# Performance work log

Hardware: AMD Instinct MI355X
Metric: run time of the kernel (lower is better)

Reference implementation:

```python
import jax, jax.numpy as jnp
import numpy as np

N_NODES = 40000
N_EDGES = 640000
N_GRAPHS = 64
F_IN = 32       # fourier_order*4
D_EMB = 256     # int(0.5*512)
D_HID = 512     # int(0.5*1024)
D_FC = 1024     # int(0.5*2048)
N_CLS = 10


def setup_inputs() -> dict:
    key = jax.random.key(0)
    ks = iter(jax.random.split(key, 40))
    rn = lambda shape, s=0.05: jax.random.normal(next(ks), shape, jnp.float32) * s
    inp = {
        'x': jax.random.normal(next(ks), (N_NODES, F_IN), jnp.float32),
        'edge_index': jax.random.randint(next(ks), (2, N_EDGES), 0, N_NODES, jnp.int32),
        'edge_attr': jax.random.uniform(next(ks), (N_EDGES, 1), jnp.float32),
        'batch': jnp.sort(jax.random.randint(next(ks), (N_NODES,), 0, N_GRAPHS, jnp.int32)),
        # embedding MLP
        'emb_w1': rn((F_IN, D_EMB)), 'emb_b1': jnp.zeros((D_EMB,), jnp.float32),
        'emb_w2': rn((D_EMB, D_EMB)), 'emb_b2': jnp.zeros((D_EMB,), jnp.float32),
        # edge_proj MLP
        'ep_w1': rn((1, 64)), 'ep_b1': jnp.zeros((64,), jnp.float32),
        'ep_w2': rn((64, 1)), 'ep_b2': jnp.zeros((1,), jnp.float32),
        # GCNConv weights (x @ W + b, PyG convention)
        'w_c1': rn((D_EMB, D_HID)), 'b_c1': jnp.zeros((D_HID,), jnp.float32),
        'w_c2': rn((D_HID, D_HID)), 'b_c2': jnp.zeros((D_HID,), jnp.float32),
        'w_c3': rn((D_HID, D_HID)), 'b_c3': jnp.zeros((D_HID,), jnp.float32),
        'w_c4': rn((D_HID, D_HID)), 'b_c4': jnp.zeros((D_HID,), jnp.float32),
        'w_c5': rn((D_HID, D_HID)), 'b_c5': jnp.zeros((D_HID,), jnp.float32),
        'w_c6': rn((D_HID, D_HID)), 'b_c6': jnp.zeros((D_HID,), jnp.float32),
        # head
        'fc1_w': rn((D_HID, D_FC)), 'fc1_b': jnp.zeros((D_FC,), jnp.float32),
        'head_w': rn((D_FC, N_CLS)), 'head_b': jnp.zeros((N_CLS,), jnp.float32),
    }
    return inp


def _gcn_conv(x, src, dst, norm, W, b):
    # PyG GCNConv: linear transform, then normalized scatter-add aggregation, then bias
    h = x @ W                                   # [N, d_out]
    msg = h[src] * norm[:, None]                # [E+N, d_out] gathered messages
    agg = jax.ops.segment_sum(msg, dst, num_segments=N_NODES)
    return agg + b


def _forward(x, edge_attr, emb_w1, emb_b1, emb_w2, emb_b2, ep_w1, ep_b1, ep_w2, ep_b2,
             w_c1, b_c1, w_c2, b_c2, w_c3, b_c3, w_c4, b_c4, w_c5, b_c5, w_c6, b_c6,
             fc1_w, fc1_b, head_w, head_b, edge_index, batch):
    # edge weights from edge_proj MLP (sigmoid output in (0,1))
    ew = jax.nn.sigmoid(jax.nn.relu(edge_attr @ ep_w1 + ep_b1) @ ep_w2 + ep_b2)[:, 0]  # [E]
    # gcn_norm with self loops (identical for every conv layer -> compute once)
    loops = jnp.arange(N_NODES, dtype=edge_index.dtype)
    src = jnp.concatenate([edge_index[0], loops])
    dst = jnp.concatenate([edge_index[1], loops])
    w = jnp.concatenate([ew, jnp.ones((N_NODES,), ew.dtype)])
    deg = jax.ops.segment_sum(w, dst, num_segments=N_NODES)
    dinv = jnp.where(deg > 0, jax.lax.rsqrt(jnp.maximum(deg, 1e-12)), 0.0)
    norm = dinv[src] * w * dinv[dst]            # [E+N]

    h = jax.nn.relu(jax.nn.relu(x @ emb_w1 + emb_b1) @ emb_w2 + emb_b2)
    h = _gcn_conv(h, src, dst, norm, w_c1, b_c1)
    skip = jax.nn.relu(h)
    h = _gcn_conv(skip, src, dst, norm, w_c2, b_c2)
    h = jax.nn.relu(h)
    h = _gcn_conv(h, src, dst, norm, w_c3, b_c3)
    skip = jax.nn.relu(h) + skip                # has_skip=True
    h = _gcn_conv(skip, src, dst, norm, w_c4, b_c4)  # is_deep=True
    h = jax.nn.relu(h)
    h = _gcn_conv(h, src, dst, norm, w_c5, b_c5)
    h = jax.nn.relu(h)
    h = _gcn_conv(h, src, dst, norm, w_c6, b_c6)
    skip = jax.nn.relu(h) + skip

    # global mean pool over graphs
    sums = jax.ops.segment_sum(skip, batch, num_segments=N_GRAPHS)
    cnts = jax.ops.segment_sum(jnp.ones((N_NODES,), skip.dtype), batch, num_segments=N_GRAPHS)
    pooled = sums / jnp.maximum(cnts, 1.0)[:, None]   # [G, D_HID]

    out = jax.nn.relu(pooled @ fc1_w + fc1_b) @ head_w + head_b   # [G, N_CLS]
    return out


def reference(x, edge_index, edge_attr, batch, emb_w1, emb_b1, emb_w2, emb_b2,
              ep_w1, ep_b1, ep_w2, ep_b2, w_c1, b_c1, w_c2, b_c2, w_c3, b_c3,
              w_c4, b_c4, w_c5, b_c5, w_c6, b_c6, fc1_w, fc1_b, head_w, head_b):
    return _forward(x, edge_attr, emb_w1, emb_b1, emb_w2, emb_b2, ep_w1, ep_b1, ep_w2, ep_b2,
                    w_c1, b_c1, w_c2, b_c2, w_c3, b_c3, w_c4, b_c4, w_c5, b_c5, w_c6, b_c6,
                    fc1_w, fc1_b, head_w, head_b, edge_index, batch)
```

## Files before the change

### kernel.cpp

```cpp
#include <hip/hip_runtime.h>
#include <math.h>

#define N_NODES 40000
#define MP      40192
#define NROWB   157
#define N_EDGES 640000
#define N_GRAPHS 64
#define F_IN 32
#define D_EMB 256
#define D_HID 512
#define D_FC 1024
#define N_CLS 10

typedef _Float16 f16x8 __attribute__((ext_vector_type(8)));
typedef float f32x4  __attribute__((ext_vector_type(4)));
typedef unsigned short u16;

template <int N> struct VecU;
template <> struct VecU<2> { typedef unsigned T __attribute__((ext_vector_type(2))); };
template <> struct VecU<4> { typedef unsigned T __attribute__((ext_vector_type(4))); };

__device__ __forceinline__ float h2f(u16 u) {
    union { u16 s; _Float16 h; } v; v.s = u; return (float)v.h;
}
__device__ __forceinline__ u16 f2h(float f) {
    union { u16 s; _Float16 h; } v; v.h = (_Float16)f; return v.s;
}
__device__ __forceinline__ void async16(void* lds, const void* g) {
    __builtin_amdgcn_global_load_lds((const __attribute__((address_space(1))) void*)g,
                                     (__attribute__((address_space(3))) void*)lds, 16, 0, 0);
}

__global__ void prep_all(const float* __restrict__ x, u16* __restrict__ xb, u16* __restrict__ G,
                         float* __restrict__ deg, int* __restrict__ cnt, int* __restrict__ cursor,
                         float* __restrict__ sums) {
    int i = blockIdx.x * blockDim.x + threadIdx.x;
    if (i < N_NODES) { deg[i] = 1.0f; cnt[i] = 0; cursor[i] = 0; }
    if (i < MP * F_IN) {
        int row = i >> 5;
        xb[i] = (row < N_NODES) ? f2h(x[i]) : (u16)0;
    }
    if (i < (MP - N_NODES) * D_HID) G[(size_t)N_NODES * D_HID + i] = 0;
    if (i < N_GRAPHS * D_HID) sums[i] = 0.f;
}

__global__ void edge_mlp_deg(const float* __restrict__ edge_attr,
                             const float* __restrict__ ep_w1, const float* __restrict__ ep_b1,
                             const float* __restrict__ ep_w2, const float* __restrict__ ep_b2,
                             const int* __restrict__ dst,
                             float* __restrict__ ew, float* __restrict__ deg, int* __restrict__ cnt) {
    __shared__ float w1[64], b1[64], w2[64];
    int t = threadIdx.x;
    if (t < 64) { w1[t] = ep_w1[t]; b1[t] = ep_b1[t]; w2[t] = ep_w2[t]; }
    __syncthreads();
    int e = blockIdx.x * blockDim.x + t;
    if (e >= N_EDGES) return;
    float x = edge_attr[e];
    float s = ep_b2[0];
#pragma unroll
    for (int j = 0; j < 64; ++j) s += fmaxf(x * w1[j] + b1[j], 0.f) * w2[j];
    float sig = 1.f / (1.f + expf(-s));
    ew[e] = sig;
    int d = dst[e];
    atomicAdd(&deg[d], sig);
    atomicAdd(&cnt[d], 1);
}

__global__ void dinv_kernel(const float* __restrict__ deg, float* __restrict__ dinv,
                            float* __restrict__ nloop) {
    int i = blockIdx.x * blockDim.x + threadIdx.x;
    if (i >= N_NODES) return;
    float d = deg[i];
    float r = (d > 0.f) ? rsqrtf(fmaxf(d, 1e-12f)) : 0.f;
    dinv[i] = r;
    nloop[i] = r * r;
}

__global__ void scan_kernel(const int* __restrict__ cnt, int* __restrict__ rowptr) {
    __shared__ int part[1024];
    int t = threadIdx.x;
    const int PER = (N_NODES + 1023) / 1024;
    int base = t * PER;
    int s = 0;
    for (int k = 0; k < PER; ++k) { int i = base + k; if (i < N_NODES) s += cnt[i]; }
    part[t] = s;
    __syncthreads();
    for (int off = 1; off < 1024; off <<= 1) {
        int v = (t >= off) ? part[t - off] : 0;
        __syncthreads();
        part[t] += v;
        __syncthreads();
    }
    int run = (t == 0) ? 0 : part[t - 1];
    for (int k = 0; k < PER; ++k) {
        int i = base + k;
        if (i < N_NODES) { rowptr[i] = run; run += cnt[i]; }
    }
    if (t == 1023) rowptr[N_NODES] = run;
}

__global__ void fill_csr_kernel(const int* __restrict__ src, const int* __restrict__ dst,
                                const float* __restrict__ ew, const float* __restrict__ dinv,
                                const int* __restrict__ rowptr, int* __restrict__ cursor,
                                int2* __restrict__ cv) {
    int e = blockIdx.x * blockDim.x + threadIdx.x;
    if (e >= N_EDGES) return;
    int d = dst[e];
    int s = src[e];
    float n = dinv[s] * ew[e] * dinv[d];
    int p = rowptr[d] + atomicAdd(&cursor[d], 1);
    cv[p] = make_int2(s, __float_as_int(n));
}

struct WPair { const float* s; u16* d; int K; int N; };
struct WP8 { WPair m[8]; };

__global__ void wprep_all(WP8 a) {
    __shared__ u16 th[32][33];
    WPair w = a.m[blockIdx.z];
    int n0 = blockIdx.x * 32;
    int k0 = blockIdx.y * 32;
    if (n0 >= w.N || k0 >= w.K) return;
    int tx = threadIdx.x, ty = threadIdx.y;
#pragma unroll
    for (int r = 0; r < 4; ++r) {
        int k = ty + r * 8;
        th[k][tx] = f2h(w.s[(size_t)(k0 + k) * w.N + n0 + tx]);
    }
    __syncthreads();
#pragma unroll
    for (int r = 0; r < 4; ++r) {
        int n = ty + r * 8;
        w.d[(size_t)(n0 + n) * w.K + k0 + tx] = th[tx][n];
    }
}

__launch_bounds__(512)
__global__ void mfma_gemm(const u16* __restrict__ A,
                          const u16* __restrict__ W,
                          const float* __restrict__ bias,
                          const u16* __restrict__ skip,
                          u16* __restrict__ C, int K, int N,
                          const int* __restrict__ batch, float* __restrict__ pool) {
    __shared__ __align__(16) u16 smem[2 * 12288];
    __shared__ int sbatch[128];

    int nColB = N >> 7;
    int b = blockIdx.x;
    int rowI = (b >> 3) / nColB * 8 + (b & 7);
    int colI = (b >> 3) % nColB;
    if (rowI >= NROWB) return;
    int rowBase = rowI * 256;
    int colBase = colI * 128;

    int t = threadIdx.x;
    int lane = t & 63;
    int wave = t >> 6;
    int wr = wave >> 1;
    int wc = wave & 1;

    int tt  = (lane & 7) ^ ((lane >> 3) & 7);
    int rrl = ((lane >> 3) << 1) | (tt >> 2);
    int sel = (tt & 3) * 8;
    int r0A = wave * 32;
    int r0W = wave * 16;

    int quad = lane >> 4;
    int mrow = lane & 15;

    const u16* gA = A + (size_t)(rowBase + r0A + rrl) * K + sel;
    const u16* gW = W + (size_t)(colBase + r0W + rrl) * K + sel;

    f32x4 acc[4][4] = {};

    int nIter = K >> 5;
    {
        u16* As = smem; u16* Ws = smem + 8192;
        async16(&As[r0A * 32], gA);
        async16(&As[(r0A + 16) * 32], gA + (size_t)16 * K);
        async16(&Ws[r0W * 32], gW);
    }

    for (int it = 0; it < nIter; ++it) {
        int cur = it & 1;
        __syncthreads();
        if (it + 1 < nIter) {
            int k0 = (it + 1) << 5;
            u16* As = smem + (cur ^ 1) * 12288; u16* Ws = As + 8192;
            async16(&As[r0A * 32], gA + k0);
            async16(&As[(r0A + 16) * 32], gA + k0 + (size_t)16 * K);
            async16(&Ws[r0W * 32], gW + k0);
        }
        const u16* As = smem + cur * 12288;
        const u16* Ws = As + 8192;
        f16x8 af[4], wf[4];
#pragma unroll
        for (int i = 0; i < 4; ++i) {
            int Ra = wr * 64 + i * 16 + mrow;
            int sa = ((Ra & 1) * 4 + quad) ^ ((Ra >> 1) & 7);
            af[i] = *(const f16x8*)&As[(Ra >> 1) * 64 + sa * 8];
            int Rb = wc * 64 + i * 16 + mrow;
            int sb = ((Rb & 1) * 4 + quad) ^ ((Rb >> 1) & 7);
            wf[i] = *(const f16x8*)&Ws[(Rb >> 1) * 64 + sb * 8];
        }
#pragma unroll
        for (int i = 0; i < 4; ++i)
#pragma unroll
            for (int j = 0; j < 4; ++j)
                acc[i][j] = __builtin_amdgcn_mfma_f32_16x16x32_f16(af[i], wf[j], acc[i][j], 0, 0, 0);
    }
    __syncthreads();

    const int ES = 132;
    u16* eb = smem;
#pragma unroll
    for (int ph = 0; ph < 2; ++ph) {
        if ((wr >> 1) == ph) {
#pragma unroll
            for (int j = 0; j < 4; ++j) {
                int col = colBase + wc * 64 + j * 16 + mrow;
                float bv = bias[col];
#pragma unroll
                for (int i = 0; i < 4; ++i) {
#pragma unroll
                    for (int r = 0; r < 4; ++r) {
                        int lr = (wr & 1) * 64 + i * 16 + quad * 4 + r;
                        size_t row = (size_t)rowBase + ph * 128 + lr;
                        float v = fmaxf(acc[i][j][r] + bv, 0.f);
                        if (skip) v += h2f(skip[row * N + col]);
                        eb[lr * ES + wc * 64 + j * 16 + mrow] = f2h(v);
                    }
                }
            }
        }
        if (pool && t < 128) {
            int row = rowBase + ph * 128 + t;
            sbatch[t] = (row < N_NODES) ? batch[row] : -1;
        }
        __syncthreads();
        if (C) {
#pragma unroll
            for (int k = 0; k < 4; ++k) {
                int c = t + k * 512;
                int row = c >> 4;
                int ch = c & 15;
                f16x8 v = *(const f16x8*)&eb[row * ES + ch * 8];
                __builtin_nontemporal_store(v,
                    (f16x8*)&C[(size_t)(rowBase + ph * 128 + row) * N + colBase + ch * 8]);
            }
        }
        if (pool) {
            int c = t & 127;
            int rs = (t >> 7) * 32;
            float run = 0.f; int g = -1;
            for (int r = rs; r < rs + 32; ++r) {
                int bg = sbatch[r];
                if (bg != g) {
                    if (g >= 0) atomicAdd(&pool[(size_t)g * D_HID + colBase + c], run);
                    run = 0.f; g = bg;
                }
                if (bg >= 0) run += h2f(eb[r * ES + c]);
            }
            if (g >= 0) atomicAdd(&pool[(size_t)g * D_HID + colBase + c], run);
        }
        __syncthreads();
    }
}

template <int D>
__launch_bounds__(256)
__global__ void gather_f16(const u16* __restrict__ h, const int* __restrict__ rowptr,
                           const int2* __restrict__ cv, const float* __restrict__ nloop,
                           u16* __restrict__ out) {
    constexpr int FPL = D / 64;
    constexpr int UPL = FPL / 2;
    using VU = typename VecU<UPL>::T;
    int node = blockIdx.x * 4 + (threadIdx.x >> 6);
    int lane = threadIdx.x & 63;
    if (node >= N_NODES) return;
    union UU { unsigned u; _Float16 h[2]; };
    float acc[FPL];
    float sl = nloop[node];
    {
        VU own = *(const VU*)(h + (size_t)node * D + lane * FPL);
#pragma unroll
        for (int u = 0; u < UPL; ++u) {
            UU w; w.u = own[u];
            acc[2 * u]     = (float)w.h[0] * sl;
            acc[2 * u + 1] = (float)w.h[1] * sl;
        }
    }
    int beg = rowptr[node], end = rowptr[node + 1];
    if (end > beg) {
        int last = end - 1;
        int2 c[8];
#pragma unroll
        for (int m = 0; m < 8; ++m) c[m] = cv[min(beg + m, last)];
        for (int j = beg; j < end; j += 8) {
            VU tv[8];
#pragma unroll
            for (int m = 0; m < 8; ++m)
                tv[m] = *(const VU*)(h + (size_t)c[m].x * D + lane * FPL);
            int jn = j + 8;
            int2 cn[8];
#pragma unroll
            for (int m = 0; m < 8; ++m) cn[m] = c[m];
            if (jn < end) {
#pragma unroll
                for (int m = 0; m < 8; ++m) cn[m] = cv[min(jn + m, last)];
            }
            __builtin_amdgcn_sched_barrier(0);
#pragma unroll
            for (int m = 0; m < 8; ++m) {
                float v = (j + m < end) ? __int_as_float(c[m].y) : 0.f;
#pragma unroll
                for (int u = 0; u < UPL; ++u) {
                    UU w; w.u = tv[m][u];
                    acc[2 * u]     += (float)w.h[0] * v;
                    acc[2 * u + 1] += (float)w.h[1] * v;
                }
            }
#pragma unroll
            for (int m = 0; m < 8; ++m) c[m] = cn[m];
        }
    }
    VU o;
#pragma unroll
    for (int u = 0; u < UPL; ++u) {
        unsigned lo = f2h(acc[2 * u]);
        unsigned hi = f2h(acc[2 * u + 1]);
        o[u] = lo | (hi << 16);
    }
    __builtin_nontemporal_store(o, (VU*)(out + (size_t)node * D + lane * FPL));
}

__launch_bounds__(256)
__global__ void fc1_head(const float* __restrict__ sums, const int* __restrict__ batch,
                         const float* __restrict__ fc1_w, const float* __restrict__ fc1_b,
                         const float* __restrict__ head_w, const float* __restrict__ head_b,
                         float* __restrict__ out) {
    __shared__ float sv[D_HID];
    __shared__ float fj[D_FC];
    __shared__ float hacc[N_CLS];
    __shared__ float invc;
    int g = blockIdx.x;
    int t = threadIdx.x;
    if (t == 0) {
        int lo = 0, hi = N_NODES;
        while (lo < hi) { int m = (lo + hi) >> 1; if (batch[m] < g) lo = m + 1; else hi = m; }
        int lb = lo;
        lo = lb; hi = N_NODES;
        while (lo < hi) { int m = (lo + hi) >> 1; if (batch[m] < g + 1) lo = m + 1; else hi = m; }
        invc = 1.f / fmaxf((float)(lo - lb), 1.f);
    }
    if (t < N_CLS) hacc[t] = 0.f;
    __syncthreads();
    for (int k = t; k < D_HID; k += 256) sv[k] = sums[(size_t)g * D_HID + k] * invc;
    __syncthreads();
#pragma unroll
    for (int m = 0; m < D_FC / 256; ++m) {
        int j = t + m * 256;
        float acc = fc1_b[j];
        for (int k = 0; k < D_HID; ++k) acc += sv[k] * fc1_w[(size_t)k * D_FC + j];
        fj[j] = fmaxf(acc, 0.f);
    }
    __syncthreads();
    float p[N_CLS] = {};
    for (int j = t; j < D_FC; j += 256) {
        float f = fj[j];
#pragma unroll
        for (int c = 0; c < N_CLS; ++c) p[c] += f * head_w[j * N_CLS + c];
    }
#pragma unroll
    for (int c = 0; c < N_CLS; ++c) {
        float v = p[c];
        for (int off = 32; off; off >>= 1) v += __shfl_down(v, off, 64);
        if ((t & 63) == 0) atomicAdd(&hacc[c], v);
    }
    __syncthreads();
    if (t < N_CLS) out[g * N_CLS + t] = hacc[t] + head_b[t];
}

extern "C" void kernel_launch(void* const* d_in, const int* in_sizes, int n_in,
                              void* d_out, int out_size, void* d_ws, size_t ws_size,
                              hipStream_t stream) {
    const float* x          = (const float*)d_in[0];
    const int*   edge_index = (const int*)d_in[1];
    const float* edge_attr  = (const float*)d_in[2];
    const int*   batch      = (const int*)d_in[3];
    const float* emb_w1 = (const float*)d_in[4];
    const float* emb_b1 = (const float*)d_in[5];
    const float* emb_w2 = (const float*)d_in[6];
    const float* emb_b2 = (const float*)d_in[7];
    const float* ep_w1  = (const float*)d_in[8];
    const float* ep_b1  = (const float*)d_in[9];
    const float* ep_w2  = (const float*)d_in[10];
    const float* ep_b2  = (const float*)d_in[11];
    const float* w_c[6] = { (const float*)d_in[12], (const float*)d_in[14], (const float*)d_in[16],
                            (const float*)d_in[18], (const float*)d_in[20], (const float*)d_in[22] };
    const float* b_c[6] = { (const float*)d_in[13], (const float*)d_in[15], (const float*)d_in[17],
                            (const float*)d_in[19], (const float*)d_in[21], (const float*)d_in[23] };
    const float* fc1_w  = (const float*)d_in[24];
    const float* fc1_b  = (const float*)d_in[25];
    const float* head_w = (const float*)d_in[26];
    const float* head_b = (const float*)d_in[27];
    float* out = (float*)d_out;

    const int* src = edge_index;
    const int* dst = edge_index + N_EDGES;

    char* p = (char*)d_ws;
    auto alloc = [&](size_t bytes) { char* r = p; p += (bytes + 255) & ~(size_t)255; return r; };
    float* ew    = (float*)alloc(N_EDGES * 4);
    float* deg   = (float*)alloc(N_NODES * 4);
    float* dinv  = (float*)alloc(N_NODES * 4);
    float* nloop = (float*)alloc(N_NODES * 4);
    int* cnt     = (int*)alloc(N_NODES * 4);
    int* cursor  = (int*)alloc(N_NODES * 4);
    int* rowptr  = (int*)alloc((N_NODES + 1) * 4);
    int2* cv     = (int2*)alloc((size_t)N_EDGES * 8);
    u16* xb = (u16*)alloc((size_t)MP * F_IN * 2);
    u16* H1 = (u16*)alloc((size_t)MP * D_EMB * 2);
    u16* H2 = (u16*)alloc((size_t)MP * D_EMB * 2);
    u16* G  = (u16*)alloc((size_t)MP * D_HID * 2);
    u16* S1 = (u16*)alloc((size_t)MP * D_HID * 2);
    u16* S2 = (u16*)alloc((size_t)MP * D_HID * 2);
    u16* Cb = (u16*)alloc((size_t)MP * D_HID * 2);
    u16* we1 = (u16*)alloc((size_t)F_IN * D_EMB * 2);
    u16* we2 = (u16*)alloc((size_t)D_EMB * D_EMB * 2);
    u16* wc[6];
    wc[0] = (u16*)alloc((size_t)D_EMB * D_HID * 2);
    for (int i = 1; i < 6; ++i) wc[i] = (u16*)alloc((size_t)D_HID * D_HID * 2);
    float* sums = (float*)alloc(N_GRAPHS * D_HID * 4);

    const int TB = 256;
    const int EB = (N_EDGES + TB - 1) / TB;
    const int NB = (N_NODES + TB - 1) / TB;

    prep_all<<<(MP * F_IN + TB - 1) / TB, TB, 0, stream>>>(x, xb, G, deg, cnt, cursor, sums);
    edge_mlp_deg<<<EB, TB, 0, stream>>>(edge_attr, ep_w1, ep_b1, ep_w2, ep_b2, dst, ew, deg, cnt);
    dinv_kernel<<<NB, TB, 0, stream>>>(deg, dinv, nloop);
    scan_kernel<<<1, 1024, 0, stream>>>(cnt, rowptr);
    fill_csr_kernel<<<EB, TB, 0, stream>>>(src, dst, ew, dinv, rowptr, cursor, cv);

    WP8 wp;
    wp.m[0] = { emb_w1, we1, F_IN,  D_EMB };
    wp.m[1] = { emb_w2, we2, D_EMB, D_EMB };
    wp.m[2] = { w_c[0], wc[0], D_EMB, D_HID };
    for (int i = 1; i < 6; ++i) wp.m[2 + i] = { w_c[i], wc[i], D_HID, D_HID };
    wprep_all<<<dim3(16, 16, 8), dim3(32, 8), 0, stream>>>(wp);

    const int SLOTS = ((NROWB + 7) / 8) * 8;
    const int GRID2 = SLOTS * (D_EMB / 128);
    const int GRID4 = SLOTS * (D_HID / 128);
    mfma_gemm<<<GRID2, 512, 0, stream>>>(xb, we1, emb_b1, nullptr, H1, F_IN, D_EMB, nullptr, nullptr);
    mfma_gemm<<<GRID2, 512, 0, stream>>>(H1, we2, emb_b2, nullptr, H2, D_EMB, D_EMB, nullptr, nullptr);

    const int GG = (N_NODES + 3) / 4;
    gather_f16<D_EMB><<<GG, 256, 0, stream>>>(H2, rowptr, cv, nloop, G);
    mfma_gemm<<<GRID4, 512, 0, stream>>>(G, wc[0], b_c[0], nullptr, S1, D_EMB, D_HID, nullptr, nullptr);
    gather_f16<D_HID><<<GG, 256, 0, stream>>>(S1, rowptr, cv, nloop, G);
    mfma_gemm<<<GRID4, 512, 0, stream>>>(G, wc[1], b_c[1], nullptr, Cb, D_HID, D_HID, nullptr, nullptr);
    gather_f16<D_HID><<<GG, 256, 0, stream>>>(Cb, rowptr, cv, nloop, G);
    mfma_gemm<<<GRID4, 512, 0, stream>>>(G, wc[2], b_c[2], S1, S2, D_HID, D_HID, nullptr, nullptr);
    gather_f16<D_HID><<<GG, 256, 0, stream>>>(S2, rowptr, cv, nloop, G);
    mfma_gemm<<<GRID4, 512, 0, stream>>>(G, wc[3], b_c[3], nullptr, Cb, D_HID, D_HID, nullptr, nullptr);
    gather_f16<D_HID><<<GG, 256, 0, stream>>>(Cb, rowptr, cv, nloop, G);
    mfma_gemm<<<GRID4, 512, 0, stream>>>(G, wc[4], b_c[4], nullptr, Cb, D_HID, D_HID, nullptr, nullptr);
    gather_f16<D_HID><<<GG, 256, 0, stream>>>(Cb, rowptr, cv, nloop, G);
    mfma_gemm<<<GRID4, 512, 0, stream>>>(G, wc[5], b_c[5], S2, nullptr, D_HID, D_HID, batch, sums);

    fc1_head<<<N_GRAPHS, 256, 0, stream>>>(sums, batch, fc1_w, fc1_b, head_w, head_b, out);
}
```

Before: 1.266 ms.

## Use explicit vmcnt waits in GEMM loop, drop nontemporal stores, widen fc1 head

The GEMM main loop swaps __syncthreads for raw s_barrier plus explicit s_waitcnt vmcnt counts, so the prefetch of the next tile can stay in flight while the current tile is consumed. Nontemporal stores in the GEMM epilogue and the gather kernel become plain stores, which may keep the freshly written activations in cache for the next kernel that reads them. The fc1/head kernel now launches 1024 threads, one per FC output, instead of looping over 256 threads. The hand-written wait counts depend on how async16 is lowered, so a wrong vmcnt could cause a race.

Measured after the change: 1.203 ms. 1.05x faster.

```diff
diff --git a/kernel.cpp b/kernel.cpp
--- a/kernel.cpp
+++ b/kernel.cpp
@@ -183,14 +183,21 @@
 
     for (int it = 0; it < nIter; ++it) {
         int cur = it & 1;
-        __syncthreads();
+        __builtin_amdgcn_s_barrier();
         if (it + 1 < nIter) {
             int k0 = (it + 1) << 5;
             u16* As = smem + (cur ^ 1) * 12288; u16* Ws = As + 8192;
             async16(&As[r0A * 32], gA + k0);
             async16(&As[(r0A + 16) * 32], gA + k0 + (size_t)16 * K);
             async16(&Ws[r0W * 32], gW + k0);
-        }
+            asm volatile("s_waitcnt vmcnt(3)" ::: "memory");
+        } else {
+            asm volatile("s_waitcnt vmcnt(0)" ::: "memory");
+        }
+        __builtin_amdgcn_sched_barrier(0);
+        __builtin_amdgcn_s_barrier();
+        __builtin_amdgcn_sched_barrier(0);
+
         const u16* As = smem + cur * 12288;
         const u16* Ws = As + 8192;
         f16x8 af[4], wf[4];
@@ -245,8 +252,7 @@
                 int row = c >> 4;
                 int ch = c & 15;
                 f16x8 v = *(const f16x8*)&eb[row * ES + ch * 8];
-                __builtin_nontemporal_store(v,
-                    (f16x8*)&C[(size_t)(rowBase + ph * 128 + row) * N + colBase + ch * 8]);
+                *(f16x8*)&C[(size_t)(rowBase + ph * 128 + row) * N + colBase + ch * 8] = v;
             }
         }
         if (pool) {
@@ -331,16 +337,15 @@
         unsigned hi = f2h(acc[2 * u + 1]);
         o[u] = lo | (hi << 16);
     }
-    __builtin_nontemporal_store(o, (VU*)(out + (size_t)node * D + lane * FPL));
-}
-
-__launch_bounds__(256)
+    *(VU*)(out + (size_t)node * D + lane * FPL) = o;
+}
+
+__launch_bounds__(1024)
 __global__ void fc1_head(const float* __restrict__ sums, const int* __restrict__ batch,
                          const float* __restrict__ fc1_w, const float* __restrict__ fc1_b,
                          const float* __restrict__ head_w, const float* __restrict__ head_b,
                          float* __restrict__ out) {
     __shared__ float sv[D_HID];
-    __shared__ float fj[D_FC];
     __shared__ float hacc[N_CLS];
     __shared__ float invc;
     int g = blockIdx.x;
@@ -355,22 +360,16 @@
     }
     if (t < N_CLS) hacc[t] = 0.f;
     __syncthreads();
-    for (int k = t; k < D_HID; k += 256) sv[k] = sums[(size_t)g * D_HID + k] * invc;
-    __syncthreads();
-#pragma unroll
-    for (int m = 0; m < D_FC / 256; ++m) {
-        int j = t + m * 256;
-        float acc = fc1_b[j];
-        for (int k = 0; k < D_HID; ++k) acc += sv[k] * fc1_w[(size_t)k * D_FC + j];
-        fj[j] = fmaxf(acc, 0.f);
-    }
-    __syncthreads();
-    float p[N_CLS] = {};
-    for (int j = t; j < D_FC; j += 256) {
-        float f = fj[j];
-#pragma unroll
-        for (int c = 0; c < N_CLS; ++c) p[c] += f * head_w[j * N_CLS + c];
-    }
+    if (t < D_HID) sv[t] = sums[(size_t)g * D_HID + t] * invc;
+    __syncthreads();
+    int j = t;
+    float acc = fc1_b[j];
+#pragma unroll 8
+    for (int k = 0; k < D_HID; ++k) acc += sv[k] * fc1_w[(size_t)k * D_FC + j];
+    float f = fmaxf(acc, 0.f);
+    float p[N_CLS];
+#pragma unroll
+    for (int c = 0; c < N_CLS; ++c) p[c] = f * head_w[j * N_CLS + c];
 #pragma unroll
     for (int c = 0; c < N_CLS; ++c) {
         float v = p[c];
@@ -470,5 +469,5 @@
     gather_f16<D_HID><<<GG, 256, 0, stream>>>(Cb, rowptr, cv, nloop, G);
     mfma_gemm<<<GRID4, 512, 0, stream>>>(G, wc[5], b_c[5], S2, nullptr, D_HID, D_HID, batch, sums);
 
-    fc1_head<<<N_GRAPHS, 256, 0, stream>>>(sums, batch, fc1_w, fc1_b, head_w, head_b, out);
-}
+    fc1_head<<<N_GRAPHS, 1024, 0, stream>>>(sums, batch, fc1_w, fc1_b, head_w, head_b, out);
+}
```
